# Kernel tuning notes

Measured on AMD Instinct MI355X. Metric: run time of the kernel, lower is better.

## Reference

```python
import jax, jax.numpy as jnp
import numpy as np

WS = 8      # window_size
NH = 8      # n_heads
EPS = 1e-06


def _rel_coords(ws):
    # Swin-style relative position index table, matches torch buffer construction
    c = np.stack(np.meshgrid(np.arange(ws), np.arange(ws), indexing='ij'))  # [2,ws,ws]
    c = c.reshape(2, -1)                      # [2, L]
    rel = c[:, :, None] - c[:, None, :]       # [2, L, L]
    rel = rel.transpose(1, 2, 0) + (ws - 1)   # [L, L, 2]
    rel[:, :, 0] *= 2 * ws - 1
    return jnp.asarray(rel.sum(-1), dtype=jnp.int32)  # [L, L]


def rms_film(x, t, gw, bw):
    # x: [B,C,H,W], t: [B,d_t]; RMS over channel dim, FiLM scale/shift from t
    g = (t @ gw.T)[:, :, None, None]
    b = (t @ bw.T)[:, :, None, None]
    return g * x * jax.lax.rsqrt(jnp.mean(x * x, axis=1, keepdims=True) + EPS) + b


def window_attn(x, wq, wk, wv, wo_w, wo_b, rpb):
    B, C, H, W = x.shape
    h, w = H // WS, W // WS
    L = WS * WS
    dh = C // NH
    # partition into windows: [B, h, w, L, C]
    xw = x.reshape(B, C, h, WS, w, WS).transpose(0, 2, 4, 3, 5, 1).reshape(B, h, w, L, C)

    def heads(p):
        y = xw @ p.T  # Linear, no bias
        return y.reshape(B, h, w, L, NH, dh).transpose(0, 1, 2, 4, 3, 5)  # [B,h,w,n,L,dh]

    q, k, v = heads(wq), heads(wk), heads(wv)
    bias = rpb[:, _rel_coords(WS)]  # [NH, L, L] gather from bias table
    attn = jnp.einsum('bhwnld,bhwnmd->bhwnlm', q, k) / float(np.sqrt(dh)) + bias
    o = jnp.einsum('bhwnlm,bhwnmd->bhwnld', jax.nn.softmax(attn, axis=-1), v)
    # merge windows, channel order (n c): [B, NH*dh, H, W]
    o = o.reshape(B, h, w, NH, WS, WS, dh).transpose(0, 3, 6, 1, 4, 2, 5).reshape(B, C, H, W)
    # 1x1 conv output projection (with bias)
    return jnp.einsum('bchw,oc->bohw', o, wo_w) + wo_b[None, :, None, None]


def convnext(x, t, dw_w, dw_b, gw, bw, w1, b1, w2, b2):
    # 7x7 depthwise conv, pad 3
    y = jax.lax.conv_general_dilated(
        x, dw_w, window_strides=(1, 1), padding=[(3, 3), (3, 3)],
        dimension_numbers=('NCHW', 'OIHW', 'NCHW'), feature_group_count=x.shape[1])
    y = y + dw_b[None, :, None, None]
    y = rms_film(y, t, gw, bw).transpose(0, 2, 3, 1)  # -> NHWC
    y = jax.nn.gelu(y @ w1.T + b1, approximate=False) @ w2.T + b2
    return y.transpose(0, 3, 1, 2)


def setup_inputs() -> dict:
    key = jax.random.key(0)
    ks = jax.random.split(key, 16)
    D, DT, B, H, W = 256, 256, 8, 128, 128
    DH = 4 * D
    n = lambda k, s: jax.random.normal(k, s, jnp.float32) * 0.02
    return dict(
        x=jax.random.normal(ks[0], (B, D, H, W), jnp.float32),
        t=jax.random.normal(ks[1], (B, DT), jnp.float32),
        an_g=n(ks[2], (D, DT)), an_b=n(ks[3], (D, DT)),
        wq=n(ks[4], (D, D)), wk=n(ks[5], (D, D)), wv=n(ks[6], (D, D)),
        wo_w=n(ks[7], (D, D)), wo_b=jnp.zeros((D,), jnp.float32),
        rpb=n(ks[8], (NH, (2 * WS - 1) ** 2)),
        dw_w=n(ks[9], (D, 1, 7, 7)), dw_b=jnp.zeros((D,), jnp.float32),
        fn_g=n(ks[10], (D, DT)), fn_b=n(ks[11], (D, DT)),
        w1=n(ks[12], (DH, D)), b1=jnp.zeros((DH,), jnp.float32),
        w2=n(ks[13], (D, DH)), b2=jnp.zeros((D,), jnp.float32))


def reference(x, t, an_g, an_b, wq, wk, wv, wo_w, wo_b, rpb,
              dw_w, dw_b, fn_g, fn_b, w1, b1, w2, b2):
    x = x + window_attn(rms_film(x, t, an_g, an_b), wq, wk, wv, wo_w, wo_b, rpb)
    return x + convnext(x, t, dw_w, dw_b, fn_g, fn_b, w1, b1, w2, b2)
```

## Files before the change

kernel.cpp:

```cpp
#include <hip/hip_runtime.h>
#include <math.h>

typedef __attribute__((ext_vector_type(8))) short bf16x8_t;
typedef __attribute__((ext_vector_type(4))) float f32x4;

__device__ __forceinline__ unsigned short f2bf(float f) {
  unsigned int u = __builtin_bit_cast(unsigned int, f);
  u += 0x7FFFu + ((u >> 16) & 1u);
  return (unsigned short)(u >> 16);
}
__device__ __forceinline__ float bf2f(unsigned short h) {
  unsigned int u = ((unsigned int)h) << 16;
  return __builtin_bit_cast(float, u);
}

typedef const __attribute__((address_space(1))) void* as1cv;
typedef __attribute__((address_space(3))) void* as3v;

__device__ __forceinline__ void gld_lds16(const unsigned short* g, unsigned short* l) {
  __builtin_amdgcn_global_load_lds((as1cv)g, (as3v)l, 16, 0, 0);
}

__global__ __launch_bounds__(256) void tvec_kernel(const float* __restrict__ t,
    const float* __restrict__ an_g, const float* __restrict__ an_b,
    const float* __restrict__ fn_g, const float* __restrict__ fn_b,
    float* __restrict__ gvec) {
  int d = threadIdx.x;
  int b = blockIdx.x;
  int m = blockIdx.y;
  __shared__ float ts[256];
  ts[d] = t[b * 256 + d];
  __syncthreads();
  const float* W = (m == 0) ? an_g : (m == 1) ? an_b : (m == 2) ? fn_g : fn_b;
  float acc = 0.f;
  #pragma unroll 8
  for (int k = 0; k < 256; ++k) acc += ts[k] * W[d * 256 + k];
  gvec[(m * 8 + b) * 256 + d] = acc;
}

__global__ __launch_bounds__(256) void wconv_kernel(const float* __restrict__ wq,
    const float* __restrict__ wk, const float* __restrict__ wv, const float* __restrict__ wo,
    const float* __restrict__ w1, const float* __restrict__ w2,
    unsigned short* __restrict__ outp) {
  int i = blockIdx.x * 256 + threadIdx.x;
  const float* src; int off;
  if      (i <  65536) { src = wq; off = 0; }
  else if (i < 131072) { src = wk; off = 65536; }
  else if (i < 196608) { src = wv; off = 131072; }
  else if (i < 262144) { src = wo; off = 196608; }
  else if (i < 524288) { src = w1; off = 262144; }
  else                 { src = w2; off = 524288; }
  outp[i] = f2bf(src[i - off]);
}

template<int IS_BF, int WX>
__global__ __launch_bounds__(256) void film_kernel(const void* __restrict__ in_,
    const float* __restrict__ gvec, int gsel, unsigned short* __restrict__ outbf,
    unsigned short* __restrict__ xbf) {
  const float* inf = (const float*)in_;
  const unsigned short* inb = (const unsigned short*)in_;
  int blk = blockIdx.x;
  int b = blk >> 8;
  int p0 = (blk & 255) << 6;
  int lane = threadIdx.x & 63;
  int cg = threadIdx.x >> 6;
  __shared__ unsigned short vals[64][264];
  __shared__ float ssred[4][64];
  __shared__ float rinvs[64];
  size_t base = ((size_t)b << 22) + p0;
  float ss = 0.f;
  #pragma unroll 4
  for (int ci = 0; ci < 64; ++ci) {
    int c = (cg << 6) + ci;
    size_t idx = base + ((size_t)c << 14) + lane;
    float v = IS_BF ? bf2f(inb[idx]) : inf[idx];
    ss += v * v;
    unsigned short hv = f2bf(v);
    vals[lane][c] = hv;
    if (WX) xbf[idx] = hv;
  }
  ssred[cg][lane] = ss;
  __syncthreads();
  if (threadIdx.x < 64) {
    float s = ssred[0][threadIdx.x] + ssred[1][threadIdx.x] + ssred[2][threadIdx.x] + ssred[3][threadIdx.x];
    rinvs[threadIdx.x] = rsqrtf(s * (1.0f / 256.0f) + 1e-6f);
  }
  __syncthreads();
  int pix = threadIdx.x >> 2;
  int c0 = (threadIdx.x & 3) << 6;
  float rv = rinvs[pix];
  const float* gp = gvec + ((gsel * 2 + 0) * 8 + b) * 256;
  const float* bp = gvec + ((gsel * 2 + 1) * 8 + b) * 256;
  unsigned short* orow = outbf + (((size_t)b << 14) + p0 + pix) * 256 + c0;
  #pragma unroll
  for (int ch = 0; ch < 8; ++ch) {
    bf16x8_t pack;
    #pragma unroll
    for (int e = 0; e < 8; ++e) {
      int c = c0 + ch * 8 + e;
      float v = bf2f(vals[pix][c]);
      float o = gp[c] * v * rv + bp[c];
      pack[e] = (short)f2bf(o);
    }
    *(bf16x8_t*)(orow + ch * 8) = pack;
  }
}

template<int DO_GELU>
__global__ __launch_bounds__(256) void gemm_kernel(const unsigned short* __restrict__ A,
    const unsigned short* __restrict__ Bw, const float* __restrict__ bias,
    unsigned short* __restrict__ outp, int K, int N) {
  __shared__ unsigned short As[128 * 64];
  __shared__ unsigned short Bs[128 * 64];
  int tid = threadIdx.x;
  int m0 = blockIdx.x << 7;
  int n0 = blockIdx.y << 7;
  int w = tid >> 6, lane = tid & 63;
  int wm = (w >> 1) << 6, wn = (w & 1) << 6;
  f32x4 acc[4][4];
  #pragma unroll
  for (int mi = 0; mi < 4; ++mi)
    #pragma unroll
    for (int ni = 0; ni < 4; ++ni)
      acc[mi][ni] = (f32x4){0.f, 0.f, 0.f, 0.f};

  for (int k0 = 0; k0 < K; k0 += 64) {
    #pragma unroll
    for (int r2 = 0; r2 < 4; ++r2) {
      int linear = (r2 << 8) + tid;
      int row = linear >> 3;
      int ch = linear & 7;
      gld_lds16(A  + (size_t)(m0 + row) * K + k0 + ch * 8, As + linear * 8);
      gld_lds16(Bw + (size_t)(n0 + row) * K + k0 + ch * 8, Bs + linear * 8);
    }
    __syncthreads();
    #pragma unroll
    for (int kk = 0; kk < 64; kk += 32) {
      bf16x8_t af[4], bq[4];
      int lr = lane & 15;
      int lk = ((lane >> 4) << 3) + kk;
      #pragma unroll
      for (int mi = 0; mi < 4; ++mi)
        af[mi] = *(const bf16x8_t*)(As + ((wm + (mi << 4) + lr) << 6) + lk);
      #pragma unroll
      for (int ni = 0; ni < 4; ++ni)
        bq[ni] = *(const bf16x8_t*)(Bs + ((wn + (ni << 4) + lr) << 6) + lk);
      #pragma unroll
      for (int mi = 0; mi < 4; ++mi)
        #pragma unroll
        for (int ni = 0; ni < 4; ++ni)
          acc[mi][ni] = __builtin_amdgcn_mfma_f32_16x16x32_bf16(af[mi], bq[ni], acc[mi][ni], 0, 0, 0);
    }
    __syncthreads();
  }
  int lr = lane & 15, lg = lane >> 4;
  #pragma unroll
  for (int mi = 0; mi < 4; ++mi) {
    #pragma unroll
    for (int ni = 0; ni < 4; ++ni) {
      int col = n0 + wn + (ni << 4) + lr;
      int row = m0 + wm + (mi << 4) + (lg << 2);
      f32x4 a = acc[mi][ni];
      #pragma unroll
      for (int i = 0; i < 4; ++i) {
        float v = a[i];
        if (DO_GELU) {
          v += bias[col];
          v = 0.5f * v * (1.0f + erff(v * 0.70710678118654752f));
        }
        outp[(size_t)(row + i) * N + col] = f2bf(v);
      }
    }
  }
}

__global__ __launch_bounds__(256) void gemm_t_kernel(const unsigned short* __restrict__ A,
    const unsigned short* __restrict__ Bw, unsigned short* __restrict__ outp) {
  __shared__ unsigned short smem[16384];
  unsigned short* As = smem;
  unsigned short* Bs = smem + 8192;
  const int K = 256;
  int tid = threadIdx.x;
  int m0 = blockIdx.x << 7;
  int n0 = blockIdx.y << 7;
  int w = tid >> 6, lane = tid & 63;
  int wm = (w >> 1) << 6, wn = (w & 1) << 6;
  f32x4 acc[4][4];
  #pragma unroll
  for (int mi = 0; mi < 4; ++mi)
    #pragma unroll
    for (int ni = 0; ni < 4; ++ni)
      acc[mi][ni] = (f32x4){0.f, 0.f, 0.f, 0.f};

  for (int k0 = 0; k0 < K; k0 += 64) {
    #pragma unroll
    for (int r2 = 0; r2 < 4; ++r2) {
      int linear = (r2 << 8) + tid;
      int row = linear >> 3;
      int ch = linear & 7;
      gld_lds16(A  + (size_t)(m0 + row) * K + k0 + ch * 8, As + linear * 8);
      gld_lds16(Bw + (size_t)(n0 + row) * K + k0 + ch * 8, Bs + linear * 8);
    }
    __syncthreads();
    #pragma unroll
    for (int kk = 0; kk < 64; kk += 32) {
      bf16x8_t af[4], bq[4];
      int lr = lane & 15;
      int lk = ((lane >> 4) << 3) + kk;
      #pragma unroll
      for (int mi = 0; mi < 4; ++mi)
        af[mi] = *(const bf16x8_t*)(As + ((wm + (mi << 4) + lr) << 6) + lk);
      #pragma unroll
      for (int ni = 0; ni < 4; ++ni)
        bq[ni] = *(const bf16x8_t*)(Bs + ((wn + (ni << 4) + lr) << 6) + lk);
      #pragma unroll
      for (int mi = 0; mi < 4; ++mi)
        #pragma unroll
        for (int ni = 0; ni < 4; ++ni)
          acc[mi][ni] = __builtin_amdgcn_mfma_f32_16x16x32_bf16(af[mi], bq[ni], acc[mi][ni], 0, 0, 0);
    }
    __syncthreads();
  }

  int lr = lane & 15, lg = lane >> 4;
  #pragma unroll
  for (int mi = 0; mi < 4; ++mi)
    #pragma unroll
    for (int ni = 0; ni < 4; ++ni) {
      int cl = wn + (ni << 4) + lr;
      int rl = wm + (mi << 4) + (lg << 2);
      f32x4 a = acc[mi][ni];
      #pragma unroll
      for (int i = 0; i < 4; ++i)
        smem[cl * 128 + rl + i] = f2bf(a[i]);
    }
  __syncthreads();

  int cl = tid >> 1;
  int half = tid & 1;
  int b = m0 >> 14;
  int pix = (m0 & 16383) + half * 64;
  int c = n0 + cl;
  const unsigned short* srow = smem + cl * 128 + half * 64;
  unsigned short* orow = outp + ((size_t)b * 256 + c) * 16384 + pix;
  #pragma unroll
  for (int jj = 0; jj < 8; ++jj)
    *(bf16x8_t*)(orow + jj * 8) = *(const bf16x8_t*)(srow + jj * 8);
}

__global__ __launch_bounds__(256) void gemm_wof_kernel(const unsigned short* __restrict__ A,
    const unsigned short* __restrict__ Bw, const float* __restrict__ bias,
    const unsigned short* __restrict__ xbf, unsigned short* __restrict__ outp) {
  __shared__ unsigned short smem[16384];
  unsigned short* As = smem;
  unsigned short* Bs = smem + 8192;
  const int K = 256;
  int tid = threadIdx.x;
  int m0 = blockIdx.x << 7;
  int n0 = blockIdx.y << 7;
  int w = tid >> 6, lane = tid & 63;
  int wm = (w >> 1) << 6, wn = (w & 1) << 6;
  f32x4 acc[4][4];
  #pragma unroll
  for (int mi = 0; mi < 4; ++mi)
    #pragma unroll
    for (int ni = 0; ni < 4; ++ni)
      acc[mi][ni] = (f32x4){0.f, 0.f, 0.f, 0.f};

  for (int k0 = 0; k0 < K; k0 += 64) {
    #pragma unroll
    for (int r2 = 0; r2 < 4; ++r2) {
      int linear = (r2 << 8) + tid;
      int row = linear >> 3;
      int ch = linear & 7;
      gld_lds16(A  + (size_t)(m0 + row) * K + k0 + ch * 8, As + linear * 8);
      gld_lds16(Bw + (size_t)(n0 + row) * K + k0 + ch * 8, Bs + linear * 8);
    }
    __syncthreads();
    #pragma unroll
    for (int kk = 0; kk < 64; kk += 32) {
      bf16x8_t af[4], bq[4];
      int lr = lane & 15;
      int lk = ((lane >> 4) << 3) + kk;
      #pragma unroll
      for (int mi = 0; mi < 4; ++mi)
        af[mi] = *(const bf16x8_t*)(As + ((wm + (mi << 4) + lr) << 6) + lk);
      #pragma unroll
      for (int ni = 0; ni < 4; ++ni)
        bq[ni] = *(const bf16x8_t*)(Bs + ((wn + (ni << 4) + lr) << 6) + lk);
      #pragma unroll
      for (int mi = 0; mi < 4; ++mi)
        #pragma unroll
        for (int ni = 0; ni < 4; ++ni)
          acc[mi][ni] = __builtin_amdgcn_mfma_f32_16x16x32_bf16(af[mi], bq[ni], acc[mi][ni], 0, 0, 0);
    }
    __syncthreads();
  }

  int lr = lane & 15, lg = lane >> 4;
  #pragma unroll
  for (int mi = 0; mi < 4; ++mi)
    #pragma unroll
    for (int ni = 0; ni < 4; ++ni) {
      int cl = wn + (ni << 4) + lr;
      int rl = wm + (mi << 4) + (lg << 2);
      f32x4 a = acc[mi][ni];
      #pragma unroll
      for (int i = 0; i < 4; ++i)
        smem[cl * 128 + rl + i] = f2bf(a[i]);
    }
  __syncthreads();

  int cl = tid >> 1;
  int half = tid & 1;
  int b = m0 >> 14;
  int pix = (m0 & 16383) + half * 64;
  int c = n0 + cl;
  const unsigned short* srow = smem + cl * 128 + half * 64;
  size_t gbase = ((size_t)b * 256 + c) * 16384 + pix;
  const unsigned short* xrow = xbf + gbase;
  unsigned short* orow = outp + gbase;
  float bb = bias[c];
  #pragma unroll
  for (int jj = 0; jj < 8; ++jj) {
    bf16x8_t sv = *(const bf16x8_t*)(srow + jj * 8);
    bf16x8_t xv = *(const bf16x8_t*)(xrow + jj * 8);
    bf16x8_t ov;
    #pragma unroll
    for (int e = 0; e < 8; ++e)
      ov[e] = (short)f2bf(bf2f((unsigned short)sv[e]) + bf2f((unsigned short)xv[e]) + bb);
    *(bf16x8_t*)(orow + jj * 8) = ov;
  }
}

__global__ __launch_bounds__(256) void gemm2f_kernel(const unsigned short* __restrict__ A,
    const unsigned short* __restrict__ Bw, const float* __restrict__ bias,
    const unsigned short* __restrict__ x1, float* __restrict__ outp, int m_base) {
  __shared__ unsigned short smem[16384];
  unsigned short* As = smem;
  unsigned short* Bs = smem + 8192;
  const int K = 1024, N = 256;
  int tid = threadIdx.x;
  int m0 = blockIdx.x << 7;
  int n0 = blockIdx.y << 7;
  int w = tid >> 6, lane = tid & 63;
  int wm = (w >> 1) << 6, wn = (w & 1) << 6;
  f32x4 acc[4][4];
  #pragma unroll
  for (int mi = 0; mi < 4; ++mi)
    #pragma unroll
    for (int ni = 0; ni < 4; ++ni)
      acc[mi][ni] = (f32x4){0.f, 0.f, 0.f, 0.f};

  for (int k0 = 0; k0 < K; k0 += 64) {
    #pragma unroll
    for (int r2 = 0; r2 < 4; ++r2) {
      int linear = (r2 << 8) + tid;
      int row = linear >> 3;
      int ch = linear & 7;
      gld_lds16(A  + (size_t)(m0 + row) * K + k0 + ch * 8, As + linear * 8);
      gld_lds16(Bw + (size_t)(n0 + row) * K + k0 + ch * 8, Bs + linear * 8);
    }
    __syncthreads();
    #pragma unroll
    for (int kk = 0; kk < 64; kk += 32) {
      bf16x8_t af[4], bq[4];
      int lr = lane & 15;
      int lk = ((lane >> 4) << 3) + kk;
      #pragma unroll
      for (int mi = 0; mi < 4; ++mi)
        af[mi] = *(const bf16x8_t*)(As + ((wm + (mi << 4) + lr) << 6) + lk);
      #pragma unroll
      for (int ni = 0; ni < 4; ++ni)
        bq[ni] = *(const bf16x8_t*)(Bs + ((wn + (ni << 4) + lr) << 6) + lk);
      #pragma unroll
      for (int mi = 0; mi < 4; ++mi)
        #pragma unroll
        for (int ni = 0; ni < 4; ++ni)
          acc[mi][ni] = __builtin_amdgcn_mfma_f32_16x16x32_bf16(af[mi], bq[ni], acc[mi][ni], 0, 0, 0);
    }
    __syncthreads();
  }

  int lr = lane & 15, lg = lane >> 4;
  #pragma unroll
  for (int mi = 0; mi < 4; ++mi)
    #pragma unroll
    for (int ni = 0; ni < 4; ++ni) {
      int cl = wn + (ni << 4) + lr;
      int rl = wm + (mi << 4) + (lg << 2);
      f32x4 a = acc[mi][ni];
      #pragma unroll
      for (int i = 0; i < 4; ++i)
        smem[cl * 128 + rl + i] = f2bf(a[i]);
    }
  __syncthreads();

  int cl = tid >> 1;
  int half = tid & 1;
  int pglob0 = m_base + m0;
  int b = pglob0 >> 14;
  int pix = (pglob0 & 16383) + half * 64;
  int c = n0 + cl;
  const unsigned short* srow = smem + cl * 128 + half * 64;
  size_t gbase = ((size_t)b * 256 + c) * 16384 + pix;
  const unsigned short* xrow = x1 + gbase;
  float* orow = outp + gbase;
  float bb = bias[c];
  #pragma unroll
  for (int jj = 0; jj < 8; ++jj) {
    bf16x8_t sv = *(const bf16x8_t*)(srow + jj * 8);
    bf16x8_t xv = *(const bf16x8_t*)(xrow + jj * 8);
    #pragma unroll
    for (int e = 0; e < 8; ++e)
      orow[jj * 8 + e] = bf2f((unsigned short)sv[e]) + bf2f((unsigned short)xv[e]) + bb;
  }
}

__global__ __launch_bounds__(256, 3) void attn_kernel(const unsigned short* __restrict__ qg,
    const unsigned short* __restrict__ kg, const unsigned short* __restrict__ vt,
    const float* __restrict__ rpb, unsigned short* __restrict__ og) {
  __shared__ float rpbf[1800];
  __shared__ unsigned short pbuf[4][64 * 72];
  int wi = (blockIdx.x & 7) * 256 + (blockIdx.x >> 3);
  int b = wi >> 8, wh = (wi >> 4) & 15, ww = wi & 15;
  int tid = threadIdx.x;
  int w = tid >> 6, lane = tid & 63;
  int g = lane >> 4, lr = lane & 15;
  for (int idx = tid; idx < 1800; idx += 256) rpbf[idx] = rpb[idx];
  __syncthreads();

  int rowpix = (wh * 8) * 128 + ww * 8;
  size_t ibase = ((size_t)b << 14) + rowpix;
  unsigned short* pb = pbuf[w];
  const float scale = 0.17677669529663689f;

  #pragma unroll 1
  for (int hh = 0; hh < 2; ++hh) {
    int h = w * 2 + hh;
    float sums[4][4];
    {
      bf16x8_t qf[4], kf[4];
      #pragma unroll
      for (int t = 0; t < 4; ++t) {
        size_t tok = ibase + (size_t)(t * 2 + (lr >> 3)) * 128 + (lr & 7);
        qf[t] = *(const bf16x8_t*)(qg + tok * 256 + h * 32 + g * 8);
        kf[t] = *(const bf16x8_t*)(kg + tok * 256 + h * 32 + g * 8);
      }
      f32x4 sacc[4][4];
      #pragma unroll
      for (int qt = 0; qt < 4; ++qt)
        #pragma unroll
        for (int kt = 0; kt < 4; ++kt)
          sacc[qt][kt] = __builtin_amdgcn_mfma_f32_16x16x32_bf16(qf[qt], kf[kt],
                           (f32x4){0.f, 0.f, 0.f, 0.f}, 0, 0, 0);
      const float* rb = &rpbf[h * 225];
      #pragma unroll
      for (int qt = 0; qt < 4; ++qt) {
        #pragma unroll
        for (int i = 0; i < 4; ++i) {
          int q = qt * 16 + g * 4 + i;
          int il = q >> 3, jl = q & 7;
          float v[4];
          #pragma unroll
          for (int kt = 0; kt < 4; ++kt) {
            int kv = kt * 16 + lr;
            v[kt] = sacc[qt][kt][i] * scale + rb[(il - (kv >> 3) + 7) * 15 + (jl - (kv & 7) + 7)];
          }
          float mx = fmaxf(fmaxf(v[0], v[1]), fmaxf(v[2], v[3]));
          mx = fmaxf(mx, __shfl_xor(mx, 1));
          mx = fmaxf(mx, __shfl_xor(mx, 2));
          mx = fmaxf(mx, __shfl_xor(mx, 4));
          mx = fmaxf(mx, __shfl_xor(mx, 8));
          float sm = 0.f;
          #pragma unroll
          for (int kt = 0; kt < 4; ++kt) { v[kt] = __expf(v[kt] - mx); sm += v[kt]; }
          sm += __shfl_xor(sm, 1);
          sm += __shfl_xor(sm, 2);
          sm += __shfl_xor(sm, 4);
          sm += __shfl_xor(sm, 8);
          sums[qt][i] = sm;
          #pragma unroll
          for (int kt = 0; kt < 4; ++kt)
            pb[q * 72 + kt * 16 + lr] = f2bf(v[kt]);
        }
      }
    }
    f32x4 oacc[4][2];
    #pragma unroll
    for (int qt = 0; qt < 4; ++qt) {
      oacc[qt][0] = (f32x4){0.f, 0.f, 0.f, 0.f};
      oacc[qt][1] = (f32x4){0.f, 0.f, 0.f, 0.f};
    }
    #pragma unroll
    for (int ks = 0; ks < 2; ++ks) {
      bf16x8_t pf[4], vf[2];
      #pragma unroll
      for (int qt = 0; qt < 4; ++qt)
        pf[qt] = *(const bf16x8_t*)(pb + (qt * 16 + lr) * 72 + ks * 32 + g * 8);
      #pragma unroll
      for (int dt = 0; dt < 2; ++dt) {
        size_t plane = (size_t)b * 256 + h * 32 + dt * 16 + lr;
        vf[dt] = *(const bf16x8_t*)(vt + (plane << 14) + rowpix + (size_t)(ks * 4 + g) * 128);
      }
      #pragma unroll
      for (int qt = 0; qt < 4; ++qt)
        #pragma unroll
        for (int dt = 0; dt < 2; ++dt)
          oacc[qt][dt] = __builtin_amdgcn_mfma_f32_16x16x32_bf16(pf[qt], vf[dt], oacc[qt][dt], 0, 0, 0);
    }
    #pragma unroll
    for (int qt = 0; qt < 4; ++qt) {
      #pragma unroll
      for (int i = 0; i < 4; ++i) {
        int q = qt * 16 + g * 4 + i;
        float inv = 1.0f / sums[qt][i];
        size_t tok = ibase + (size_t)(q >> 3) * 128 + (q & 7);
        #pragma unroll
        for (int dt = 0; dt < 2; ++dt)
          og[tok * 256 + h * 32 + dt * 16 + lr] = f2bf(oacc[qt][dt][i] * inv);
      }
    }
  }
}

__global__ __launch_bounds__(256) void dwconv_kernel(const unsigned short* __restrict__ x1,
    const float* __restrict__ w, const float* __restrict__ bias, unsigned short* __restrict__ outp) {
  int bc = blockIdx.y;
  int c = bc & 255;
  int y0 = blockIdx.x << 6;
  __shared__ unsigned short tile[70 * 144];
  __shared__ float wf[49];
  const unsigned short* plane = x1 + ((size_t)bc << 14);
  int tid = threadIdx.x;

  for (int idx = tid; idx < 70 * 16; idx += 256) {
    int row = idx >> 4, ch = idx & 15;
    int gy = y0 - 3 + row;
    bf16x8_t v = (bf16x8_t){0, 0, 0, 0, 0, 0, 0, 0};
    if (gy >= 0 && gy < 128) v = *(const bf16x8_t*)(plane + gy * 128 + ch * 8);
    *(bf16x8_t*)(&tile[row * 144 + 8 + ch * 8]) = v;
  }
  for (int idx = tid; idx < 70 * 6; idx += 256) {
    int row = idx / 6, e = idx % 6;
    int col = (e < 3) ? (5 + e) : (133 + e);
    tile[row * 144 + col] = 0;
  }
  if (tid < 49) wf[tid] = w[c * 49 + tid];
  __syncthreads();

  int r = tid >> 2;
  int c0 = (tid & 3) << 5;
  float acc[32];
  float bb = bias[c];
  #pragma unroll
  for (int i = 0; i < 32; ++i) acc[i] = bb;

  #pragma unroll
  for (int u = 0; u < 7; ++u) {
    const unsigned short* rowp = &tile[(r + u) * 144 + c0];
    float f[48];
    #pragma unroll
    for (int k = 0; k < 6; ++k) {
      bf16x8_t v = *(const bf16x8_t*)(rowp + k * 8);
      #pragma unroll
      for (int e = 0; e < 8; ++e) f[k * 8 + e] = bf2f((unsigned short)v[e]);
    }
    #pragma unroll
    for (int t = 0; t < 7; ++t) {
      float wv = wf[u * 7 + t];
      #pragma unroll
      for (int i = 0; i < 32; ++i) acc[i] += f[i + 5 + t] * wv;
    }
  }

  unsigned short* orow = outp + ((size_t)bc << 14) + (size_t)(y0 + r) * 128 + c0;
  #pragma unroll
  for (int k = 0; k < 4; ++k) {
    bf16x8_t v;
    #pragma unroll
    for (int e = 0; e < 8; ++e) v[e] = (short)f2bf(acc[k * 8 + e]);
    *(bf16x8_t*)(orow + k * 8) = v;
  }
}

extern "C" void kernel_launch(void* const* d_in, const int* in_sizes, int n_in,
                              void* d_out, int out_size, void* d_ws, size_t ws_size,
                              hipStream_t stream) {
  const float* x    = (const float*)d_in[0];
  const float* t    = (const float*)d_in[1];
  const float* an_g = (const float*)d_in[2];
  const float* an_b = (const float*)d_in[3];
  const float* wq   = (const float*)d_in[4];
  const float* wk   = (const float*)d_in[5];
  const float* wv   = (const float*)d_in[6];
  const float* wo_w = (const float*)d_in[7];
  const float* wo_b = (const float*)d_in[8];
  const float* rpb  = (const float*)d_in[9];
  const float* dw_w = (const float*)d_in[10];
  const float* dw_b = (const float*)d_in[11];
  const float* fn_g = (const float*)d_in[12];
  const float* fn_b = (const float*)d_in[13];
  const float* w1   = (const float*)d_in[14];
  const float* b1   = (const float*)d_in[15];
  const float* w2   = (const float*)d_in[16];
  const float* b2   = (const float*)d_in[17];
  float* outp = (float*)d_out;

  char* ws = (char*)d_ws;
  const size_t MB = 1024ull * 1024ull;
  float* gvec = (float*)ws;
  unsigned short* wbf = (unsigned short*)(ws + 32768);
  unsigned short* P = (unsigned short*)(ws + 2 * MB);
  unsigned short* Q = (unsigned short*)(ws + 66 * MB);
  unsigned short* R = (unsigned short*)(ws + 130 * MB);
  unsigned short* xbf  = (unsigned short*)d_out;
  unsigned short* vbuf = (unsigned short*)((char*)d_out + 64 * MB);

  unsigned short* wq_bf = wbf;
  unsigned short* wk_bf = wbf + 65536;
  unsigned short* wv_bf = wbf + 131072;
  unsigned short* wo_bf = wbf + 196608;
  unsigned short* w1_bf = wbf + 262144;
  unsigned short* w2_bf = wbf + 524288;

  tvec_kernel<<<dim3(8, 4), 256, 0, stream>>>(t, an_g, an_b, fn_g, fn_b, gvec);
  wconv_kernel<<<3072, 256, 0, stream>>>(wq, wk, wv, wo_w, w1, w2, wbf);

  film_kernel<0, 1><<<2048, 256, 0, stream>>>(x, gvec, 0, P, xbf);

  gemm_kernel<0><<<dim3(1024, 2), 256, 0, stream>>>(P, wq_bf, nullptr, Q, 256, 256);
  gemm_kernel<0><<<dim3(1024, 2), 256, 0, stream>>>(P, wk_bf, nullptr, R, 256, 256);
  gemm_t_kernel<<<dim3(1024, 2), 256, 0, stream>>>(P, wv_bf, vbuf);

  attn_kernel<<<2048, 256, 0, stream>>>(Q, R, vbuf, rpb, P);

  gemm_wof_kernel<<<dim3(1024, 2), 256, 0, stream>>>(P, wo_bf, wo_b, xbf, R);

  dwconv_kernel<<<dim3(2, 2048), 256, 0, stream>>>(R, dw_w, dw_b, Q);
  film_kernel<1, 0><<<2048, 256, 0, stream>>>(Q, gvec, 1, P, nullptr);

  for (int qtr = 0; qtr < 4; ++qtr) {
    int m_base = qtr * 32768;
    gemm_kernel<1><<<dim3(256, 8), 256, 0, stream>>>(P + (size_t)m_base * 256, w1_bf, b1, Q, 256, 1024);
    gemm2f_kernel<<<dim3(256, 2), 256, 0, stream>>>(Q, w2_bf, b2, R, outp, m_base);
  }
}
```

Measured before the change: 936.6 us.

## Fuse Q/K/V projections into one GEMM launch and stream attention per query tile

Merges the three separate Q, K and V projection GEMM launches into a single launch with six column blocks, relying on wq/wk/wv being stored contiguously in the bf16 weight buffer. Each block routes its output to Q, K, or the transposed V buffer depending on its column offset. The attention kernel now processes one 16-row query tile at a time, which shrinks the per-wave probability buffer and register use and allows a higher occupancy bound. The trade-off is more serialized per-tile work and reloading of shared data inside the tile loop.

```diff
diff --git a/kernel.cpp b/kernel.cpp
--- a/kernel.cpp
+++ b/kernel.cpp
@@ -174,8 +174,9 @@
   }
 }
 
-__global__ __launch_bounds__(256) void gemm_t_kernel(const unsigned short* __restrict__ A,
-    const unsigned short* __restrict__ Bw, unsigned short* __restrict__ outp) {
+__global__ __launch_bounds__(256) void gemm_qkv_kernel(const unsigned short* __restrict__ A,
+    const unsigned short* __restrict__ Bw, unsigned short* __restrict__ outq,
+    unsigned short* __restrict__ outk, unsigned short* __restrict__ outvt) {
   __shared__ unsigned short smem[16384];
   unsigned short* As = smem;
   unsigned short* Bs = smem + 8192;
@@ -223,29 +224,44 @@
   }
 
   int lr = lane & 15, lg = lane >> 4;
-  #pragma unroll
-  for (int mi = 0; mi < 4; ++mi)
-    #pragma unroll
-    for (int ni = 0; ni < 4; ++ni) {
-      int cl = wn + (ni << 4) + lr;
-      int rl = wm + (mi << 4) + (lg << 2);
-      f32x4 a = acc[mi][ni];
-      #pragma unroll
-      for (int i = 0; i < 4; ++i)
-        smem[cl * 128 + rl + i] = f2bf(a[i]);
-    }
-  __syncthreads();
-
-  int cl = tid >> 1;
-  int half = tid & 1;
-  int b = m0 >> 14;
-  int pix = (m0 & 16383) + half * 64;
-  int c = n0 + cl;
-  const unsigned short* srow = smem + cl * 128 + half * 64;
-  unsigned short* orow = outp + ((size_t)b * 256 + c) * 16384 + pix;
-  #pragma unroll
-  for (int jj = 0; jj < 8; ++jj)
-    *(bf16x8_t*)(orow + jj * 8) = *(const bf16x8_t*)(srow + jj * 8);
+  if (n0 < 512) {
+    unsigned short* dst = (n0 < 256) ? outq : outk;
+    #pragma unroll
+    for (int mi = 0; mi < 4; ++mi) {
+      #pragma unroll
+      for (int ni = 0; ni < 4; ++ni) {
+        int col = (n0 & 255) + wn + (ni << 4) + lr;
+        int row = m0 + wm + (mi << 4) + (lg << 2);
+        f32x4 a = acc[mi][ni];
+        #pragma unroll
+        for (int i = 0; i < 4; ++i)
+          dst[(size_t)(row + i) * 256 + col] = f2bf(a[i]);
+      }
+    }
+  } else {
+    #pragma unroll
+    for (int mi = 0; mi < 4; ++mi)
+      #pragma unroll
+      for (int ni = 0; ni < 4; ++ni) {
+        int cl = wn + (ni << 4) + lr;
+        int rl = wm + (mi << 4) + (lg << 2);
+        f32x4 a = acc[mi][ni];
+        #pragma unroll
+        for (int i = 0; i < 4; ++i)
+          smem[cl * 128 + rl + i] = f2bf(a[i]);
+      }
+    __syncthreads();
+    int cl = tid >> 1;
+    int half = tid & 1;
+    int b = m0 >> 14;
+    int pix = (m0 & 16383) + half * 64;
+    int c = (n0 - 512) + cl;
+    const unsigned short* srow = smem + cl * 128 + half * 64;
+    unsigned short* orow = outvt + ((size_t)b * 256 + c) * 16384 + pix;
+    #pragma unroll
+    for (int jj = 0; jj < 8; ++jj)
+      *(bf16x8_t*)(orow + jj * 8) = *(const bf16x8_t*)(srow + jj * 8);
+  }
 }
 
 __global__ __launch_bounds__(256) void gemm_wof_kernel(const unsigned short* __restrict__ A,
@@ -417,11 +433,11 @@
   }
 }
 
-__global__ __launch_bounds__(256, 3) void attn_kernel(const unsigned short* __restrict__ qg,
+__global__ __launch_bounds__(256, 4) void attn_kernel(const unsigned short* __restrict__ qg,
     const unsigned short* __restrict__ kg, const unsigned short* __restrict__ vt,
     const float* __restrict__ rpb, unsigned short* __restrict__ og) {
   __shared__ float rpbf[1800];
-  __shared__ unsigned short pbuf[4][64 * 72];
+  __shared__ unsigned short pbuf[4][16 * 72];
   int wi = (blockIdx.x & 7) * 256 + (blockIdx.x >> 3);
   int b = wi >> 8, wh = (wi >> 4) & 15, ww = wi & 15;
   int tid = threadIdx.x;
@@ -438,87 +454,74 @@
   #pragma unroll 1
   for (int hh = 0; hh < 2; ++hh) {
     int h = w * 2 + hh;
-    float sums[4][4];
-    {
-      bf16x8_t qf[4], kf[4];
-      #pragma unroll
-      for (int t = 0; t < 4; ++t) {
-        size_t tok = ibase + (size_t)(t * 2 + (lr >> 3)) * 128 + (lr & 7);
-        qf[t] = *(const bf16x8_t*)(qg + tok * 256 + h * 32 + g * 8);
-        kf[t] = *(const bf16x8_t*)(kg + tok * 256 + h * 32 + g * 8);
-      }
-      f32x4 sacc[4][4];
-      #pragma unroll
-      for (int qt = 0; qt < 4; ++qt)
-        #pragma unroll
-        for (int kt = 0; kt < 4; ++kt)
-          sacc[qt][kt] = __builtin_amdgcn_mfma_f32_16x16x32_bf16(qf[qt], kf[kt],
-                           (f32x4){0.f, 0.f, 0.f, 0.f}, 0, 0, 0);
-      const float* rb = &rpbf[h * 225];
-      #pragma unroll
-      for (int qt = 0; qt < 4; ++qt) {
-        #pragma unroll
-        for (int i = 0; i < 4; ++i) {
-          int q = qt * 16 + g * 4 + i;
-          int il = q >> 3, jl = q & 7;
-          float v[4];
-          #pragma unroll
-          for (int kt = 0; kt < 4; ++kt) {
-            int kv = kt * 16 + lr;
-            v[kt] = sacc[qt][kt][i] * scale + rb[(il - (kv >> 3) + 7) * 15 + (jl - (kv & 7) + 7)];
-          }
-          float mx = fmaxf(fmaxf(v[0], v[1]), fmaxf(v[2], v[3]));
-          mx = fmaxf(mx, __shfl_xor(mx, 1));
-          mx = fmaxf(mx, __shfl_xor(mx, 2));
-          mx = fmaxf(mx, __shfl_xor(mx, 4));
-          mx = fmaxf(mx, __shfl_xor(mx, 8));
-          float sm = 0.f;
-          #pragma unroll
-          for (int kt = 0; kt < 4; ++kt) { v[kt] = __expf(v[kt] - mx); sm += v[kt]; }
-          sm += __shfl_xor(sm, 1);
-          sm += __shfl_xor(sm, 2);
-          sm += __shfl_xor(sm, 4);
-          sm += __shfl_xor(sm, 8);
-          sums[qt][i] = sm;
-          #pragma unroll
-          for (int kt = 0; kt < 4; ++kt)
-            pb[q * 72 + kt * 16 + lr] = f2bf(v[kt]);
-        }
-      }
-    }
-    f32x4 oacc[4][2];
-    #pragma unroll
-    for (int qt = 0; qt < 4; ++qt) {
-      oacc[qt][0] = (f32x4){0.f, 0.f, 0.f, 0.f};
-      oacc[qt][1] = (f32x4){0.f, 0.f, 0.f, 0.f};
-    }
-    #pragma unroll
-    for (int ks = 0; ks < 2; ++ks) {
-      bf16x8_t pf[4], vf[2];
-      #pragma unroll
-      for (int qt = 0; qt < 4; ++qt)
-        pf[qt] = *(const bf16x8_t*)(pb + (qt * 16 + lr) * 72 + ks * 32 + g * 8);
+    bf16x8_t qf[4], kf[4];
+    #pragma unroll
+    for (int t = 0; t < 4; ++t) {
+      size_t tok = ibase + (size_t)(t * 2 + (lr >> 3)) * 128 + (lr & 7);
+      qf[t] = *(const bf16x8_t*)(qg + tok * 256 + h * 32 + g * 8);
+      kf[t] = *(const bf16x8_t*)(kg + tok * 256 + h * 32 + g * 8);
+    }
+    bf16x8_t vfr[2][2];
+    #pragma unroll
+    for (int ks = 0; ks < 2; ++ks)
       #pragma unroll
       for (int dt = 0; dt < 2; ++dt) {
         size_t plane = (size_t)b * 256 + h * 32 + dt * 16 + lr;
-        vf[dt] = *(const bf16x8_t*)(vt + (plane << 14) + rowpix + (size_t)(ks * 4 + g) * 128);
+        vfr[ks][dt] = *(const bf16x8_t*)(vt + (plane << 14) + rowpix + (size_t)(ks * 4 + g) * 128);
       }
-      #pragma unroll
-      for (int qt = 0; qt < 4; ++qt)
-        #pragma unroll
-        for (int dt = 0; dt < 2; ++dt)
-          oacc[qt][dt] = __builtin_amdgcn_mfma_f32_16x16x32_bf16(pf[qt], vf[dt], oacc[qt][dt], 0, 0, 0);
-    }
-    #pragma unroll
+    const float* rb = &rpbf[h * 225];
+
+    #pragma unroll 1
     for (int qt = 0; qt < 4; ++qt) {
+      f32x4 sacc[4];
+      #pragma unroll
+      for (int kt = 0; kt < 4; ++kt)
+        sacc[kt] = __builtin_amdgcn_mfma_f32_16x16x32_bf16(qf[qt], kf[kt],
+                     (f32x4){0.f, 0.f, 0.f, 0.f}, 0, 0, 0);
+      float sums[4];
       #pragma unroll
       for (int i = 0; i < 4; ++i) {
         int q = qt * 16 + g * 4 + i;
-        float inv = 1.0f / sums[qt][i];
+        int il = q >> 3, jl = q & 7;
+        float v[4];
+        #pragma unroll
+        for (int kt = 0; kt < 4; ++kt) {
+          int kv = kt * 16 + lr;
+          v[kt] = sacc[kt][i] * scale + rb[(il - (kv >> 3) + 7) * 15 + (jl - (kv & 7) + 7)];
+        }
+        float mx = fmaxf(fmaxf(v[0], v[1]), fmaxf(v[2], v[3]));
+        mx = fmaxf(mx, __shfl_xor(mx, 1));
+        mx = fmaxf(mx, __shfl_xor(mx, 2));
+        mx = fmaxf(mx, __shfl_xor(mx, 4));
+        mx = fmaxf(mx, __shfl_xor(mx, 8));
+        float sm = 0.f;
+        #pragma unroll
+        for (int kt = 0; kt < 4; ++kt) { v[kt] = __expf(v[kt] - mx); sm += v[kt]; }
+        sm += __shfl_xor(sm, 1);
+        sm += __shfl_xor(sm, 2);
+        sm += __shfl_xor(sm, 4);
+        sm += __shfl_xor(sm, 8);
+        sums[i] = sm;
+        #pragma unroll
+        for (int kt = 0; kt < 4; ++kt)
+          pb[(g * 4 + i) * 72 + kt * 16 + lr] = f2bf(v[kt]);
+      }
+      f32x4 oacc[2] = {(f32x4){0.f, 0.f, 0.f, 0.f}, (f32x4){0.f, 0.f, 0.f, 0.f}};
+      #pragma unroll
+      for (int ks = 0; ks < 2; ++ks) {
+        bf16x8_t pf = *(const bf16x8_t*)(pb + lr * 72 + ks * 32 + g * 8);
+        oacc[0] = __builtin_amdgcn_mfma_f32_16x16x32_bf16(pf, vfr[ks][0], oacc[0], 0, 0, 0);
+        oacc[1] = __builtin_amdgcn_mfma_f32_16x16x32_bf16(pf, vfr[ks][1], oacc[1], 0, 0, 0);
+      }
+      #pragma unroll
+      for (int i = 0; i < 4; ++i) {
+        int q = qt * 16 + g * 4 + i;
+        float inv = 1.0f / sums[i];
         size_t tok = ibase + (size_t)(q >> 3) * 128 + (q & 7);
-        #pragma unroll
-        for (int dt = 0; dt < 2; ++dt)
-          og[tok * 256 + h * 32 + dt * 16 + lr] = f2bf(oacc[qt][dt][i] * inv);
+        unsigned int packed0 = f2bf(oacc[0][i] * inv);
+        unsigned int packed1 = f2bf(oacc[1][i] * inv);
+        og[tok * 256 + h * 32 + lr] = (unsigned short)packed0;
+        og[tok * 256 + h * 32 + 16 + lr] = (unsigned short)packed1;
       }
     }
   }
@@ -617,9 +620,6 @@
   unsigned short* xbf  = (unsigned short*)d_out;
   unsigned short* vbuf = (unsigned short*)((char*)d_out + 64 * MB);
 
-  unsigned short* wq_bf = wbf;
-  unsigned short* wk_bf = wbf + 65536;
-  unsigned short* wv_bf = wbf + 131072;
   unsigned short* wo_bf = wbf + 196608;
   unsigned short* w1_bf = wbf + 262144;
   unsigned short* w2_bf = wbf + 524288;
@@ -629,9 +629,7 @@
 
   film_kernel<0, 1><<<2048, 256, 0, stream>>>(x, gvec, 0, P, xbf);
 
-  gemm_kernel<0><<<dim3(1024, 2), 256, 0, stream>>>(P, wq_bf, nullptr, Q, 256, 256);
-  gemm_kernel<0><<<dim3(1024, 2), 256, 0, stream>>>(P, wk_bf, nullptr, R, 256, 256);
-  gemm_t_kernel<<<dim3(1024, 2), 256, 0, stream>>>(P, wv_bf, vbuf);
+  gemm_qkv_kernel<<<dim3(1024, 6), 256, 0, stream>>>(P, wbf, Q, R, vbuf);
 
   attn_kernel<<<2048, 256, 0, stream>>>(Q, R, vbuf, rpb, P);
 
```

After: 984.9 us. +5.2%, slower.
